# Performance work log

Measured on AMD Instinct MI355X. Metric: run time of the kernel, lower is better.

The kernel has to match this reference:

```python
import jax, jax.numpy as jnp
import numpy as np

EPS_LEN = 1e-20
EPS_DENOM = 1e-6


def _dot(a, b):
    return jnp.sum(a * b, axis=-1, keepdims=True)


def _safe_normalize(x):
    return x / jnp.sqrt(jnp.maximum(_dot(x, x), EPS_LEN))


def _auto_normals(positions, faces):
    i0, i1, i2 = faces[:, 0], faces[:, 1], faces[:, 2]
    v0 = positions[i0]
    v1 = positions[i1]
    v2 = positions[i2]
    face_normals = jnp.cross(v1 - v0, v2 - v0)  # [F,3]
    v_nrm = jnp.zeros_like(positions)
    v_nrm = v_nrm.at[i0].add(face_normals)
    v_nrm = v_nrm.at[i1].add(face_normals)
    v_nrm = v_nrm.at[i2].add(face_normals)
    default = jnp.array([0.0, 0.0, 1.0], dtype=positions.dtype)
    v_nrm = jnp.where(_dot(v_nrm, v_nrm) > EPS_LEN, v_nrm, default)
    return _safe_normalize(v_nrm)


def _compute_tangents(positions, normals, faces, texcoords, uv_faces):
    pos = [positions[faces[:, i]] for i in range(3)]
    tex = [texcoords[uv_faces[:, i]] for i in range(3)]
    uve1 = tex[1] - tex[0]
    uve2 = tex[2] - tex[0]
    pe1 = pos[1] - pos[0]
    pe2 = pos[2] - pos[0]
    nom = pe1 * uve2[..., 1:2] - pe2 * uve1[..., 1:2]  # [F,3]
    denom = uve1[..., 0:1] * uve2[..., 1:2] - uve1[..., 1:2] * uve2[..., 0:1]
    denom = jnp.where(denom > 0.0,
                      jnp.maximum(denom, EPS_DENOM),
                      jnp.minimum(denom, -EPS_DENOM))
    tang = nom / denom  # [F,3]
    tangents = jnp.zeros_like(normals)
    for i in range(3):
        tangents = tangents.at[faces[:, i]].add(tang)
    tangents = _safe_normalize(tangents)
    tangents = _safe_normalize(tangents - _dot(tangents, normals) * normals)
    return tangents


def setup_inputs() -> dict:
    key = jax.random.key(0)
    k1, k2, k3, k4 = jax.random.split(key, 4)
    V, T, F = 2_000_000, 2_200_000, 4_000_000
    positions = jax.random.normal(k1, (V, 3), dtype=jnp.float32)
    faces = jax.random.randint(k2, (F, 3), 0, V, dtype=jnp.int32)
    texcoords = jax.random.uniform(k3, (T, 2), dtype=jnp.float32)
    uv_faces = jax.random.randint(k4, (F, 3), 0, T, dtype=jnp.int32)
    return {"positions": positions, "faces": faces,
            "texcoords": texcoords, "uv_faces": uv_faces}


def reference(positions, faces, texcoords, uv_faces):
    normals = _auto_normals(positions, faces)
    tangents = _compute_tangents(positions, normals, faces, texcoords, uv_faces)
    return jnp.stack([normals, tangents])  # [2, V, 3]
```

## Files before the change

### kernel.cpp

```cpp
#include <hip/hip_runtime.h>

#define EPS_LEN   1e-20f
#define EPS_DENOM 1e-6f

#define BLKA     1024

#define CBF_LOG  10
#define CBF      (1 << CBF_LOG)
#define NBCP     2048
#define CAPF     7168
#define FST      6

#define CB2_LOG  13
#define CB2      (1 << CB2_LOG)
#define MAXB2    256
#define CAP2     57344
#define QLOG     11
#define QSIZE    (1 << QLOG)

__global__ __launch_bounds__(BLKA)
void vg_face_bin_f(const float* __restrict__ pos, const int* __restrict__ faces,
                   const float* __restrict__ tex, const int* __restrict__ uvf,
                   float* __restrict__ face_data, unsigned* __restrict__ E,
                   int* __restrict__ cursors, int* __restrict__ validw,
                   float* __restrict__ nacc, float* __restrict__ tacc,
                   int F, int NBC)
{
    __shared__ int h[NBCP];
    __shared__ int s0[NBCP];
    __shared__ int s1[NBCP];
    __shared__ int lfill[NBCP];
    __shared__ unsigned       spack[3 * BLKA];
    __shared__ unsigned short sbuck[3 * BLKA];

    const int t = threadIdx.x;
    const int f = blockIdx.x * BLKA + t;

    h[t] = 0; h[t + 1024] = 0;
    lfill[t] = 0; lfill[t + 1024] = 0;
    for (int i = t; i < 3 * BLKA; i += BLKA) sbuck[i] = 0xFFFFu;
    __syncthreads();

    const bool on = (f < F);
    int i0 = 0, i1 = 0, i2 = 0;
    float nx = 0, ny = 0, nz = 0, txv = 0, tyv = 0, tzv = 0;

    if (on) {
        i0 = faces[3 * f + 0]; i1 = faces[3 * f + 1]; i2 = faces[3 * f + 2];

        const float p0x = pos[3*i0+0], p0y = pos[3*i0+1], p0z = pos[3*i0+2];
        const float p1x = pos[3*i1+0], p1y = pos[3*i1+1], p1z = pos[3*i1+2];
        const float p2x = pos[3*i2+0], p2y = pos[3*i2+1], p2z = pos[3*i2+2];

        const float e1x = p1x - p0x, e1y = p1y - p0y, e1z = p1z - p0z;
        const float e2x = p2x - p0x, e2y = p2y - p0y, e2z = p2z - p0z;

        nx = e1y * e2z - e1z * e2y;
        ny = e1z * e2x - e1x * e2z;
        nz = e1x * e2y - e1y * e2x;

        const int t0 = uvf[3 * f + 0];
        const int t1 = uvf[3 * f + 1];
        const int t2 = uvf[3 * f + 2];

        const float u0x = tex[2*t0+0], u0y = tex[2*t0+1];
        const float u1x = tex[2*t1+0], u1y = tex[2*t1+1];
        const float u2x = tex[2*t2+0], u2y = tex[2*t2+1];

        const float d1x = u1x - u0x, d1y = u1y - u0y;
        const float d2x = u2x - u0x, d2y = u2y - u0y;

        float denom = d1x * d2y - d1y * d2x;
        denom = (denom > 0.0f) ? fmaxf(denom, EPS_DENOM) : fminf(denom, -EPS_DENOM);
        const float inv = 1.0f / denom;

        txv = (e1x * d2y - e2x * d1y) * inv;
        tyv = (e1y * d2y - e2y * d1y) * inv;
        tzv = (e1z * d2y - e2z * d1y) * inv;

        float* fd = &face_data[(size_t)f * FST];
        reinterpret_cast<float2*>(fd)[0] = make_float2(nx, ny);
        reinterpret_cast<float2*>(fd)[1] = make_float2(nz, txv);
        reinterpret_cast<float2*>(fd)[2] = make_float2(tyv, tzv);

        atomicAdd(&h[i0 >> CBF_LOG], 1);
        atomicAdd(&h[i1 >> CBF_LOG], 1);
        atomicAdd(&h[i2 >> CBF_LOG], 1);
    }
    __syncthreads();

    s0[t] = h[t]; s0[t + 1024] = h[t + 1024];
    __syncthreads();
    int* src = s0; int* dst = s1;
    for (int d = 1; d < NBCP; d <<= 1) {
        dst[t] = src[t] + ((t >= d) ? src[t - d] : 0);
        const int k = t + 1024;
        dst[k] = src[k] + ((k >= d) ? src[k - d] : 0);
        __syncthreads();
        int* tmp = src; src = dst; dst = tmp;
    }
    int* loffp  = dst;
    int* gbasep = h;
    for (int k = t; k < NBCP; k += 1024) {
        const int incl = src[k];
        const int cnt  = h[k];
        const int lo   = incl - cnt;
        int gb = -1;
        if (k < NBC && cnt > 0) {
            gb = atomicAdd(&cursors[k], cnt);
            if (gb + cnt <= CAPF) atomicMax(&validw[k], gb + cnt);
            else gb = -1;
        }
        loffp[k]  = lo;
        gbasep[k] = gb;
    }
    __syncthreads();

    if (on) {
        const int vi[3] = { i0, i1, i2 };
#pragma unroll
        for (int c = 0; c < 3; ++c) {
            const int v = vi[c];
            const int b = v >> CBF_LOG;
            if (gbasep[b] >= 0) {
                const int slot = atomicAdd(&lfill[b], 1);
                const int p = loffp[b] + slot;
                spack[p] = ((unsigned)(v & (CBF - 1)) << 22) | (unsigned)f;
                sbuck[p] = (unsigned short)b;
            } else {
                atomicAdd(&nacc[3*v+0], nx);
                atomicAdd(&nacc[3*v+1], ny);
                atomicAdd(&nacc[3*v+2], nz);
                atomicAdd(&tacc[3*v+0], txv);
                atomicAdd(&tacc[3*v+1], tyv);
                atomicAdd(&tacc[3*v+2], tzv);
            }
        }
    }
    __syncthreads();

    for (int i = t; i < 3 * BLKA; i += BLKA) {
        const unsigned b = sbuck[i];
        if (b != 0xFFFFu) {
            const int g = gbasep[b] + (i - loffp[b]);
            E[(size_t)b * CAPF + g] = spack[i];
        }
    }
}

__global__ __launch_bounds__(512)
void vg_gather_reduce_f(const float* __restrict__ face_data,
                        const unsigned* __restrict__ E,
                        const int* __restrict__ validw,
                        float* __restrict__ nacc, float* __restrict__ tacc,
                        int V)
{
    __shared__ float accn[CBF * 3];
    __shared__ float acct[CBF * 3];
    const int b = blockIdx.x;
    const int t = threadIdx.x;

    for (int i = t; i < CBF * 3; i += 512) { accn[i] = 0.0f; acct[i] = 0.0f; }
    __syncthreads();

    int count = validw[b];
    if (count > CAPF) count = CAPF;
    const size_t ebase = (size_t)b * CAPF;

    for (int e = t; e < count; e += 512) {
        const unsigned ent = E[ebase + e];
        const int f    = (int)(ent & 0x3FFFFFu);
        const int vloc = (int)(ent >> 22);
        const float* fd = &face_data[(size_t)f * FST];
        const float2 a0 = reinterpret_cast<const float2*>(fd)[0];
        const float2 a1 = reinterpret_cast<const float2*>(fd)[1];
        const float2 a2 = reinterpret_cast<const float2*>(fd)[2];
        float* an = &accn[vloc * 3];
        float* at = &acct[vloc * 3];
        atomicAdd(an + 0, a0.x);
        atomicAdd(an + 1, a0.y);
        atomicAdd(an + 2, a1.x);
        atomicAdd(at + 0, a1.y);
        atomicAdd(at + 1, a2.x);
        atomicAdd(at + 2, a2.y);
    }
    __syncthreads();

    const int vbase = b << CBF_LOG;
#pragma unroll
    for (int k = 0; k < CBF; k += 512) {
        const int i = t + k;
        const int v = vbase + i;
        if (v < V) {
            float nx = nacc[3*v+0] + accn[3*i+0];
            float ny = nacc[3*v+1] + accn[3*i+1];
            float nz = nacc[3*v+2] + accn[3*i+2];
            float tx = tacc[3*v+0] + acct[3*i+0];
            float ty = tacc[3*v+1] + acct[3*i+1];
            float tz = tacc[3*v+2] + acct[3*i+2];

            const float nd = nx*nx + ny*ny + nz*nz;
            if (nd > EPS_LEN) {
                const float invn = 1.0f / sqrtf(nd);
                nx *= invn; ny *= invn; nz *= invn;
            } else {
                nx = 0.0f; ny = 0.0f; nz = 1.0f;
            }

            const float td = tx*tx + ty*ty + tz*tz;
            const float invt = 1.0f / sqrtf(fmaxf(td, EPS_LEN));
            tx *= invt; ty *= invt; tz *= invt;

            const float dp = tx*nx + ty*ny + tz*nz;
            tx -= dp * nx; ty -= dp * ny; tz -= dp * nz;

            const float td2 = tx*tx + ty*ty + tz*tz;
            const float invt2 = 1.0f / sqrtf(fmaxf(td2, EPS_LEN));
            tx *= invt2; ty *= invt2; tz *= invt2;

            nacc[3*v+0] = nx; nacc[3*v+1] = ny; nacc[3*v+2] = nz;
            tacc[3*v+0] = tx; tacc[3*v+1] = ty; tacc[3*v+2] = tz;
        }
    }
}

__global__ __launch_bounds__(BLKA)
void vg_face_bin3(const float* __restrict__ pos, const int* __restrict__ faces,
                  const float* __restrict__ tex, const int* __restrict__ uvf,
                  float* __restrict__ face_data,
                  unsigned* __restrict__ ef, unsigned short* __restrict__ ev,
                  int* __restrict__ cursors, int* __restrict__ validw,
                  float* __restrict__ nacc, float* __restrict__ tacc,
                  int F, int NBC)
{
    __shared__ int h[MAXB2], sc[MAXB2], loff[MAXB2], lfill[MAXB2], gbase[MAXB2];
    __shared__ unsigned       sface[3 * BLKA];
    __shared__ unsigned short svloc[3 * BLKA];
    __shared__ unsigned char  sbuck[3 * BLKA];

    const int t = threadIdx.x;
    const int f = blockIdx.x * BLKA + t;

    if (t < MAXB2) { h[t] = 0; lfill[t] = 0; }
    for (int i = t; i < 3 * BLKA; i += BLKA) sbuck[i] = 0xFF;
    __syncthreads();

    const bool on = (f < F);
    int i0 = 0, i1 = 0, i2 = 0;
    float nx = 0, ny = 0, nz = 0, txv = 0, tyv = 0, tzv = 0;

    if (on) {
        i0 = faces[3 * f + 0]; i1 = faces[3 * f + 1]; i2 = faces[3 * f + 2];

        const float p0x = pos[3*i0+0], p0y = pos[3*i0+1], p0z = pos[3*i0+2];
        const float p1x = pos[3*i1+0], p1y = pos[3*i1+1], p1z = pos[3*i1+2];
        const float p2x = pos[3*i2+0], p2y = pos[3*i2+1], p2z = pos[3*i2+2];

        const float e1x = p1x - p0x, e1y = p1y - p0y, e1z = p1z - p0z;
        const float e2x = p2x - p0x, e2y = p2y - p0y, e2z = p2z - p0z;

        nx = e1y * e2z - e1z * e2y;
        ny = e1z * e2x - e1x * e2z;
        nz = e1x * e2y - e1y * e2x;

        const int t0 = uvf[3 * f + 0];
        const int t1 = uvf[3 * f + 1];
        const int t2 = uvf[3 * f + 2];

        const float u0x = tex[2*t0+0], u0y = tex[2*t0+1];
        const float u1x = tex[2*t1+0], u1y = tex[2*t1+1];
        const float u2x = tex[2*t2+0], u2y = tex[2*t2+1];

        const float d1x = u1x - u0x, d1y = u1y - u0y;
        const float d2x = u2x - u0x, d2y = u2y - u0y;

        float denom = d1x * d2y - d1y * d2x;
        denom = (denom > 0.0f) ? fmaxf(denom, EPS_DENOM) : fminf(denom, -EPS_DENOM);
        const float inv = 1.0f / denom;

        txv = (e1x * d2y - e2x * d1y) * inv;
        tyv = (e1y * d2y - e2y * d1y) * inv;
        tzv = (e1z * d2y - e2z * d1y) * inv;

        float* fd = &face_data[(size_t)f * FST];
        reinterpret_cast<float2*>(fd)[0] = make_float2(nx, ny);
        reinterpret_cast<float2*>(fd)[1] = make_float2(nz, txv);
        reinterpret_cast<float2*>(fd)[2] = make_float2(tyv, tzv);

        atomicAdd(&h[i0 >> CB2_LOG], 1);
        atomicAdd(&h[i1 >> CB2_LOG], 1);
        atomicAdd(&h[i2 >> CB2_LOG], 1);
    }
    __syncthreads();

    if (t < MAXB2) sc[t] = h[t];
    __syncthreads();
    for (int d = 1; d < MAXB2; d <<= 1) {
        int v2 = 0;
        if (t < MAXB2) v2 = sc[t] + ((t >= d) ? sc[t - d] : 0);
        __syncthreads();
        if (t < MAXB2) sc[t] = v2;
        __syncthreads();
    }
    if (t < MAXB2) {
        loff[t] = sc[t] - h[t];
        const int cnt = h[t];
        int gb = -1;
        if (t < NBC && cnt > 0) {
            gb = atomicAdd(&cursors[t], cnt);
            if (gb + cnt <= CAP2) atomicMax(&validw[t], gb + cnt);
            else gb = -1;
        }
        gbase[t] = gb;
    }
    __syncthreads();

    if (on) {
        const int vi[3] = { i0, i1, i2 };
#pragma unroll
        for (int c = 0; c < 3; ++c) {
            const int v = vi[c];
            const int b = v >> CB2_LOG;
            if (gbase[b] >= 0) {
                const int slot = atomicAdd(&lfill[b], 1);
                const int p = loff[b] + slot;
                sface[p] = (unsigned)f;
                svloc[p] = (unsigned short)(v & (CB2 - 1));
                sbuck[p] = (unsigned char)b;
            } else {
                atomicAdd(&nacc[3*v+0], nx);
                atomicAdd(&nacc[3*v+1], ny);
                atomicAdd(&nacc[3*v+2], nz);
                atomicAdd(&tacc[3*v+0], txv);
                atomicAdd(&tacc[3*v+1], tyv);
                atomicAdd(&tacc[3*v+2], tzv);
            }
        }
    }
    __syncthreads();

    for (int i = t; i < 3 * BLKA; i += BLKA) {
        const unsigned b = sbuck[i];
        if (b != 0xFFu) {
            const int g = gbase[b] + (i - loff[b]);
            const size_t base = (size_t)b * CAP2;
            ef[base + g] = sface[i];
            ev[base + g] = svloc[i];
        }
    }
}

__global__ __launch_bounds__(BLKA)
void vg_bucket_reduce3(const float* __restrict__ face_data,
                       const unsigned* __restrict__ ef,
                       const unsigned short* __restrict__ ev,
                       const int* __restrict__ validw,
                       float* __restrict__ nacc, float* __restrict__ tacc,
                       int V)
{
    __shared__ float acc[QSIZE * 6];
    const int b = blockIdx.x;
    const int t = threadIdx.x;
    int count = validw[b];
    if (count > CAP2) count = CAP2;
    const size_t ebase = (size_t)b * CAP2;
    const int vbase = b << CB2_LOG;

    for (int q = 0; q < 4; ++q) {
        for (int i = t; i < QSIZE * 6; i += BLKA) acc[i] = 0.0f;
        __syncthreads();

        for (int e = t; e < count; e += BLKA) {
            const int vloc = (int)ev[ebase + e];
            if ((vloc >> QLOG) == q) {
                const unsigned f = ef[ebase + e];
                const float* fd = &face_data[(size_t)f * FST];
                const float2 a0 = reinterpret_cast<const float2*>(fd)[0];
                const float2 a1 = reinterpret_cast<const float2*>(fd)[1];
                const float2 a2 = reinterpret_cast<const float2*>(fd)[2];
                float* a = &acc[(vloc & (QSIZE - 1)) * 6];
                atomicAdd(a + 0, a0.x);
                atomicAdd(a + 1, a0.y);
                atomicAdd(a + 2, a1.x);
                atomicAdd(a + 3, a1.y);
                atomicAdd(a + 4, a2.x);
                atomicAdd(a + 5, a2.y);
            }
        }
        __syncthreads();

        for (int i = t; i < QSIZE; i += BLKA) {
            const int v = vbase + (q << QLOG) + i;
            if (v < V) {
                float nx = nacc[3*v+0] + acc[i*6+0];
                float ny = nacc[3*v+1] + acc[i*6+1];
                float nz = nacc[3*v+2] + acc[i*6+2];
                float tx = tacc[3*v+0] + acc[i*6+3];
                float ty = tacc[3*v+1] + acc[i*6+4];
                float tz = tacc[3*v+2] + acc[i*6+5];

                const float nd = nx*nx + ny*ny + nz*nz;
                if (nd > EPS_LEN) {
                    const float invn = 1.0f / sqrtf(nd);
                    nx *= invn; ny *= invn; nz *= invn;
                } else {
                    nx = 0.0f; ny = 0.0f; nz = 1.0f;
                }

                const float td = tx*tx + ty*ty + tz*tz;
                const float invt = 1.0f / sqrtf(fmaxf(td, EPS_LEN));
                tx *= invt; ty *= invt; tz *= invt;

                const float dp = tx*nx + ty*ny + tz*nz;
                tx -= dp * nx; ty -= dp * ny; tz -= dp * nz;

                const float td2 = tx*tx + ty*ty + tz*tz;
                const float invt2 = 1.0f / sqrtf(fmaxf(td2, EPS_LEN));
                tx *= invt2; ty *= invt2; tz *= invt2;

                nacc[3*v+0] = nx; nacc[3*v+1] = ny; nacc[3*v+2] = nz;
                tacc[3*v+0] = tx; tacc[3*v+1] = ty; tacc[3*v+2] = tz;
            }
        }
        __syncthreads();
    }
}

__global__ void vg_face_kernel(const float* __restrict__ pos,
                               const int*   __restrict__ faces,
                               const float* __restrict__ tex,
                               const int*   __restrict__ uvf,
                               float* __restrict__ nacc,
                               float* __restrict__ tacc,
                               int F) {
    int f = blockIdx.x * blockDim.x + threadIdx.x;
    if (f >= F) return;

    const int i0 = faces[3*f+0], i1 = faces[3*f+1], i2 = faces[3*f+2];

    const float p0x = pos[3*i0+0], p0y = pos[3*i0+1], p0z = pos[3*i0+2];
    const float p1x = pos[3*i1+0], p1y = pos[3*i1+1], p1z = pos[3*i1+2];
    const float p2x = pos[3*i2+0], p2y = pos[3*i2+1], p2z = pos[3*i2+2];

    const float e1x = p1x - p0x, e1y = p1y - p0y, e1z = p1z - p0z;
    const float e2x = p2x - p0x, e2y = p2y - p0y, e2z = p2z - p0z;

    const float nx = e1y*e2z - e1z*e2y;
    const float ny = e1z*e2x - e1x*e2z;
    const float nz = e1x*e2y - e1y*e2x;

    const int t0 = uvf[3*f+0], t1 = uvf[3*f+1], t2 = uvf[3*f+2];

    const float u0x = tex[2*t0+0], u0y = tex[2*t0+1];
    const float u1x = tex[2*t1+0], u1y = tex[2*t1+1];
    const float u2x = tex[2*t2+0], u2y = tex[2*t2+1];

    const float d1x = u1x - u0x, d1y = u1y - u0y;
    const float d2x = u2x - u0x, d2y = u2y - u0y;

    float denom = d1x * d2y - d1y * d2x;
    denom = (denom > 0.0f) ? fmaxf(denom, EPS_DENOM) : fminf(denom, -EPS_DENOM);
    const float inv = 1.0f / denom;

    const float tx = (e1x*d2y - e2x*d1y) * inv;
    const float ty = (e1y*d2y - e2y*d1y) * inv;
    const float tz = (e1z*d2y - e2z*d1y) * inv;

    atomicAdd(&nacc[3*i0+0], nx); atomicAdd(&nacc[3*i0+1], ny); atomicAdd(&nacc[3*i0+2], nz);
    atomicAdd(&nacc[3*i1+0], nx); atomicAdd(&nacc[3*i1+1], ny); atomicAdd(&nacc[3*i1+2], nz);
    atomicAdd(&nacc[3*i2+0], nx); atomicAdd(&nacc[3*i2+1], ny); atomicAdd(&nacc[3*i2+2], nz);
    atomicAdd(&tacc[3*i0+0], tx); atomicAdd(&tacc[3*i0+1], ty); atomicAdd(&tacc[3*i0+2], tz);
    atomicAdd(&tacc[3*i1+0], tx); atomicAdd(&tacc[3*i1+1], ty); atomicAdd(&tacc[3*i1+2], tz);
    atomicAdd(&tacc[3*i2+0], tx); atomicAdd(&tacc[3*i2+1], ty); atomicAdd(&tacc[3*i2+2], tz);
}

__global__ void vg_finalize_kernel(float* __restrict__ nacc,
                                   float* __restrict__ tacc,
                                   int V) {
    int v = blockIdx.x * blockDim.x + threadIdx.x;
    if (v >= V) return;

    float nx = nacc[3*v+0], ny = nacc[3*v+1], nz = nacc[3*v+2];
    float nd = nx*nx + ny*ny + nz*nz;
    if (nd > EPS_LEN) {
        const float invn = 1.0f / sqrtf(nd);
        nx *= invn; ny *= invn; nz *= invn;
    } else {
        nx = 0.0f; ny = 0.0f; nz = 1.0f;
    }

    float tx = tacc[3*v+0], ty = tacc[3*v+1], tz = tacc[3*v+2];
    float td = tx*tx + ty*ty + tz*tz;
    float invt = 1.0f / sqrtf(fmaxf(td, EPS_LEN));
    tx *= invt; ty *= invt; tz *= invt;
    const float dp = tx*nx + ty*ny + tz*nz;
    tx -= dp*nx; ty -= dp*ny; tz -= dp*nz;
    float td2 = tx*tx + ty*ty + tz*tz;
    float invt2 = 1.0f / sqrtf(fmaxf(td2, EPS_LEN));
    tx *= invt2; ty *= invt2; tz *= invt2;

    nacc[3*v+0] = nx; nacc[3*v+1] = ny; nacc[3*v+2] = nz;
    tacc[3*v+0] = tx; tacc[3*v+1] = ty; tacc[3*v+2] = tz;
}

extern "C" void kernel_launch(void* const* d_in, const int* in_sizes, int n_in,
                              void* d_out, int out_size, void* d_ws, size_t ws_size,
                              hipStream_t stream) {
    const float* pos   = (const float*)d_in[0];
    const int*   faces = (const int*)  d_in[1];
    const float* tex   = (const float*)d_in[2];
    const int*   uvf   = (const int*)  d_in[3];

    const int V = in_sizes[0] / 3;
    const int F = in_sizes[1] / 3;

    float* out  = (float*)d_out;
    float* nacc = out;
    float* tacc = out + (size_t)3 * V;

    hipMemsetAsync(d_out, 0, (size_t)out_size * sizeof(float), stream);

    const int NBC1 = (V + CBF - 1) >> CBF_LOG;
    {
        const size_t face_b = ((size_t)F * FST * sizeof(float) + 255) & ~(size_t)255;
        const size_t E_b    = ((size_t)NBC1 * CAPF * sizeof(unsigned) + 255) & ~(size_t)255;
        const size_t cur_b  = ((size_t)NBC1 * sizeof(int) + 255) & ~(size_t)255;
        const size_t need1  = face_b + E_b + 2 * cur_b + 256;

        if (ws_size >= need1 && NBC1 <= NBCP && F <= (1 << 22)) {
            char* ws = (char*)d_ws;
            float*    face_data = (float*)ws;    ws += face_b;
            unsigned* E         = (unsigned*)ws; ws += E_b;
            int*      cursors   = (int*)ws;      ws += cur_b;
            int*      validw    = (int*)ws;

            hipMemsetAsync(cursors, 0, cur_b, stream);
            hipMemsetAsync(validw,  0, cur_b, stream);

            vg_face_bin_f<<<(F + BLKA - 1) / BLKA, BLKA, 0, stream>>>(
                pos, faces, tex, uvf, face_data, E, cursors, validw,
                nacc, tacc, F, NBC1);
            vg_gather_reduce_f<<<NBC1, 512, 0, stream>>>(
                face_data, E, validw, nacc, tacc, V);
            return;
        }
    }

    const int NBC2 = (V + CB2 - 1) >> CB2_LOG;
    {
        const size_t NE2    = (size_t)NBC2 * CAP2;
        const size_t face_b = ((size_t)F * FST * sizeof(float) + 255) & ~(size_t)255;
        const size_t ef_b   = (NE2 * 4 + 255) & ~(size_t)255;
        const size_t ev2_b  = (NE2 * 2 + 255) & ~(size_t)255;
        const size_t cur_b  = ((size_t)NBC2 * sizeof(int) + 255) & ~(size_t)255;
        const size_t need2  = face_b + ef_b + ev2_b + 2 * cur_b + 256;

        if (ws_size >= need2 && NBC2 <= 255 && F < (1 << 22)) {
            char* ws = (char*)d_ws;
            float*          face_data = (float*)ws;          ws += face_b;
            unsigned*       ef        = (unsigned*)ws;       ws += ef_b;
            unsigned short* ev        = (unsigned short*)ws; ws += ev2_b;
            int*            cursors   = (int*)ws;            ws += cur_b;
            int*            validw    = (int*)ws;

            hipMemsetAsync(cursors, 0, cur_b, stream);
            hipMemsetAsync(validw,  0, cur_b, stream);

            vg_face_bin3<<<(F + BLKA - 1) / BLKA, BLKA, 0, stream>>>(
                pos, faces, tex, uvf, face_data, ef, ev, cursors, validw,
                nacc, tacc, F, NBC2);
            vg_bucket_reduce3<<<NBC2, BLKA, 0, stream>>>(
                face_data, ef, ev, validw, nacc, tacc, V);
            return;
        }
    }

    const int BLK = 256;
    vg_face_kernel<<<(F + BLK - 1) / BLK, BLK, 0, stream>>>(pos, faces, tex, uvf,
                                                            nacc, tacc, F);
    vg_finalize_kernel<<<(V + BLK - 1) / BLK, BLK, 0, stream>>>(nacc, tacc, V);
}
```

Before: 920.1 us.

## Pad per-face records to float4 pairs, prefetch entries, skip global accumulator reads

Per-face data is now stored as two float4 records (32 bytes padded) instead of three float2 writes, so the scatter and the gather each use two 16-byte accesses. The gather loop software-prefetches the next bin entry, and a global overflow flag lets the reduce skip reading nacc/tacc when no face fell back to global atomics. The bin capacity CAPF is lowered, and the two cursor/valid memsets are merged into one. In exchange, face-data bandwidth and footprint grow by a third, the lower capacity makes overflow to the global-atomic path more likely, and the overflow flag adds an atomicOr on that path.

```diff
diff --git a/kernel.cpp b/kernel.cpp
--- a/kernel.cpp
+++ b/kernel.cpp
@@ -8,23 +8,24 @@
 #define CBF_LOG  10
 #define CBF      (1 << CBF_LOG)
 #define NBCP     2048
-#define CAPF     7168
-#define FST      6
+#define CAPF     6656
 
 #define CB2_LOG  13
 #define CB2      (1 << CB2_LOG)
 #define MAXB2    256
 #define CAP2     57344
+#define FST2     6
 #define QLOG     11
 #define QSIZE    (1 << QLOG)
 
 __global__ __launch_bounds__(BLKA)
-void vg_face_bin_f(const float* __restrict__ pos, const int* __restrict__ faces,
-                   const float* __restrict__ tex, const int* __restrict__ uvf,
-                   float* __restrict__ face_data, unsigned* __restrict__ E,
-                   int* __restrict__ cursors, int* __restrict__ validw,
-                   float* __restrict__ nacc, float* __restrict__ tacc,
-                   int F, int NBC)
+void vg_face_bin_f8(const float* __restrict__ pos, const int* __restrict__ faces,
+                    const float* __restrict__ tex, const int* __restrict__ uvf,
+                    float4* __restrict__ fd4, unsigned* __restrict__ E,
+                    int* __restrict__ cursors, int* __restrict__ validw,
+                    int* __restrict__ ovfp,
+                    float* __restrict__ nacc, float* __restrict__ tacc,
+                    int F, int NBC)
 {
     __shared__ int h[NBCP];
     __shared__ int s0[NBCP];
@@ -78,10 +79,8 @@
         tyv = (e1y * d2y - e2y * d1y) * inv;
         tzv = (e1z * d2y - e2z * d1y) * inv;
 
-        float* fd = &face_data[(size_t)f * FST];
-        reinterpret_cast<float2*>(fd)[0] = make_float2(nx, ny);
-        reinterpret_cast<float2*>(fd)[1] = make_float2(nz, txv);
-        reinterpret_cast<float2*>(fd)[2] = make_float2(tyv, tzv);
+        fd4[2 * (size_t)f]     = make_float4(nx, ny, nz, txv);
+        fd4[2 * (size_t)f + 1] = make_float4(tyv, tzv, 0.0f, 0.0f);
 
         atomicAdd(&h[i0 >> CBF_LOG], 1);
         atomicAdd(&h[i1 >> CBF_LOG], 1);
@@ -128,6 +127,7 @@
                 spack[p] = ((unsigned)(v & (CBF - 1)) << 22) | (unsigned)f;
                 sbuck[p] = (unsigned short)b;
             } else {
+                atomicOr(ovfp, 1);
                 atomicAdd(&nacc[3*v+0], nx);
                 atomicAdd(&nacc[3*v+1], ny);
                 atomicAdd(&nacc[3*v+2], nz);
@@ -149,11 +149,12 @@
 }
 
 __global__ __launch_bounds__(512)
-void vg_gather_reduce_f(const float* __restrict__ face_data,
-                        const unsigned* __restrict__ E,
-                        const int* __restrict__ validw,
-                        float* __restrict__ nacc, float* __restrict__ tacc,
-                        int V)
+void vg_gather_reduce_f8(const float4* __restrict__ fd4,
+                         const unsigned* __restrict__ E,
+                         const int* __restrict__ validw,
+                         const int* __restrict__ ovfp,
+                         float* __restrict__ nacc, float* __restrict__ tacc,
+                         int V)
 {
     __shared__ float accn[CBF * 3];
     __shared__ float acct[CBF * 3];
@@ -167,37 +168,48 @@
     if (count > CAPF) count = CAPF;
     const size_t ebase = (size_t)b * CAPF;
 
-    for (int e = t; e < count; e += 512) {
-        const unsigned ent = E[ebase + e];
-        const int f    = (int)(ent & 0x3FFFFFu);
+    int e = t;
+    bool have = (e < count);
+    unsigned ent = have ? E[ebase + e] : 0u;
+    while (have) {
+        const int e2 = e + 512;
+        const bool have2 = (e2 < count);
+        const unsigned ent2 = have2 ? E[ebase + e2] : 0u;
+
+        const int fidx = (int)(ent & 0x3FFFFFu);
         const int vloc = (int)(ent >> 22);
-        const float* fd = &face_data[(size_t)f * FST];
-        const float2 a0 = reinterpret_cast<const float2*>(fd)[0];
-        const float2 a1 = reinterpret_cast<const float2*>(fd)[1];
-        const float2 a2 = reinterpret_cast<const float2*>(fd)[2];
+        const float4 ra = fd4[2 * (size_t)fidx];
+        const float4 rb = fd4[2 * (size_t)fidx + 1];
         float* an = &accn[vloc * 3];
         float* at = &acct[vloc * 3];
-        atomicAdd(an + 0, a0.x);
-        atomicAdd(an + 1, a0.y);
-        atomicAdd(an + 2, a1.x);
-        atomicAdd(at + 0, a1.y);
-        atomicAdd(at + 1, a2.x);
-        atomicAdd(at + 2, a2.y);
-    }
-    __syncthreads();
-
+        atomicAdd(an + 0, ra.x);
+        atomicAdd(an + 1, ra.y);
+        atomicAdd(an + 2, ra.z);
+        atomicAdd(at + 0, ra.w);
+        atomicAdd(at + 1, rb.x);
+        atomicAdd(at + 2, rb.y);
+
+        e = e2; ent = ent2; have = have2;
+    }
+    __syncthreads();
+
+    const int ovf = *ovfp;
     const int vbase = b << CBF_LOG;
 #pragma unroll
     for (int k = 0; k < CBF; k += 512) {
         const int i = t + k;
         const int v = vbase + i;
         if (v < V) {
-            float nx = nacc[3*v+0] + accn[3*i+0];
-            float ny = nacc[3*v+1] + accn[3*i+1];
-            float nz = nacc[3*v+2] + accn[3*i+2];
-            float tx = tacc[3*v+0] + acct[3*i+0];
-            float ty = tacc[3*v+1] + acct[3*i+1];
-            float tz = tacc[3*v+2] + acct[3*i+2];
+            float nx = accn[3*i+0];
+            float ny = accn[3*i+1];
+            float nz = accn[3*i+2];
+            float tx = acct[3*i+0];
+            float ty = acct[3*i+1];
+            float tz = acct[3*i+2];
+            if (ovf) {
+                nx += nacc[3*v+0]; ny += nacc[3*v+1]; nz += nacc[3*v+2];
+                tx += tacc[3*v+0]; ty += tacc[3*v+1]; tz += tacc[3*v+2];
+            }
 
             const float nd = nx*nx + ny*ny + nz*nz;
             if (nd > EPS_LEN) {
@@ -282,7 +294,7 @@
         tyv = (e1y * d2y - e2y * d1y) * inv;
         tzv = (e1z * d2y - e2z * d1y) * inv;
 
-        float* fd = &face_data[(size_t)f * FST];
+        float* fd = &face_data[(size_t)f * FST2];
         reinterpret_cast<float2*>(fd)[0] = make_float2(nx, ny);
         reinterpret_cast<float2*>(fd)[1] = make_float2(nz, txv);
         reinterpret_cast<float2*>(fd)[2] = make_float2(tyv, tzv);
@@ -374,7 +386,7 @@
             const int vloc = (int)ev[ebase + e];
             if ((vloc >> QLOG) == q) {
                 const unsigned f = ef[ebase + e];
-                const float* fd = &face_data[(size_t)f * FST];
+                const float* fd = &face_data[(size_t)f * FST2];
                 const float2 a0 = reinterpret_cast<const float2*>(fd)[0];
                 const float2 a1 = reinterpret_cast<const float2*>(fd)[1];
                 const float2 a2 = reinterpret_cast<const float2*>(fd)[2];
@@ -522,26 +534,26 @@
 
     const int NBC1 = (V + CBF - 1) >> CBF_LOG;
     {
-        const size_t face_b = ((size_t)F * FST * sizeof(float) + 255) & ~(size_t)255;
+        const size_t face_b = ((size_t)F * 8 * sizeof(float) + 255) & ~(size_t)255;
         const size_t E_b    = ((size_t)NBC1 * CAPF * sizeof(unsigned) + 255) & ~(size_t)255;
-        const size_t cur_b  = ((size_t)NBC1 * sizeof(int) + 255) & ~(size_t)255;
+        const size_t cur_b  = ((size_t)(NBC1 + 1) * sizeof(int) + 255) & ~(size_t)255;
         const size_t need1  = face_b + E_b + 2 * cur_b + 256;
 
         if (ws_size >= need1 && NBC1 <= NBCP && F <= (1 << 22)) {
             char* ws = (char*)d_ws;
-            float*    face_data = (float*)ws;    ws += face_b;
-            unsigned* E         = (unsigned*)ws; ws += E_b;
-            int*      cursors   = (int*)ws;      ws += cur_b;
-            int*      validw    = (int*)ws;
-
-            hipMemsetAsync(cursors, 0, cur_b, stream);
-            hipMemsetAsync(validw,  0, cur_b, stream);
-
-            vg_face_bin_f<<<(F + BLKA - 1) / BLKA, BLKA, 0, stream>>>(
-                pos, faces, tex, uvf, face_data, E, cursors, validw,
+            float4*   fd4     = (float4*)ws;     ws += face_b;
+            unsigned* E       = (unsigned*)ws;   ws += E_b;
+            int*      cursors = (int*)ws;        ws += cur_b;
+            int*      validw  = (int*)ws;
+            int*      ovfp    = validw + NBC1;
+
+            hipMemsetAsync(cursors, 0, 2 * cur_b, stream);
+
+            vg_face_bin_f8<<<(F + BLKA - 1) / BLKA, BLKA, 0, stream>>>(
+                pos, faces, tex, uvf, fd4, E, cursors, validw, ovfp,
                 nacc, tacc, F, NBC1);
-            vg_gather_reduce_f<<<NBC1, 512, 0, stream>>>(
-                face_data, E, validw, nacc, tacc, V);
+            vg_gather_reduce_f8<<<NBC1, 512, 0, stream>>>(
+                fd4, E, validw, ovfp, nacc, tacc, V);
             return;
         }
     }
@@ -549,7 +561,7 @@
     const int NBC2 = (V + CB2 - 1) >> CB2_LOG;
     {
         const size_t NE2    = (size_t)NBC2 * CAP2;
-        const size_t face_b = ((size_t)F * FST * sizeof(float) + 255) & ~(size_t)255;
+        const size_t face_b = ((size_t)F * FST2 * sizeof(float) + 255) & ~(size_t)255;
         const size_t ef_b   = (NE2 * 4 + 255) & ~(size_t)255;
         const size_t ev2_b  = (NE2 * 2 + 255) & ~(size_t)255;
         const size_t cur_b  = ((size_t)NBC2 * sizeof(int) + 255) & ~(size_t)255;
```

After: 921.7 us. About the same (+0.2%).
